# Kernel optimization log

Hardware: AMD Instinct MI355X
Metric: run time of the kernel (lower is better)

The kernel has to match this reference:

```python
import jax, jax.numpy as jnp
import numpy as np

NUM_TAGS = 256
BATCH = 64
SEQ = 512


def setup_inputs() -> dict:
    key = jax.random.key(0)
    k1, k2, k3 = jax.random.split(key, 3)
    logits = jax.random.normal(k1, (BATCH, SEQ, NUM_TAGS), dtype=jnp.float32)
    tags = jax.random.randint(k2, (BATCH, SEQ), 0, NUM_TAGS, dtype=jnp.int32)
    mask = jnp.ones((BATCH, SEQ), dtype=jnp.int32)
    # learned parameter: transitions [K, K] (xavier-normal-ish init)
    std = float(np.sqrt(2.0 / (NUM_TAGS + NUM_TAGS)))
    transitions = jax.random.normal(k3, (NUM_TAGS, NUM_TAGS), dtype=jnp.float32) * std
    return {"logits": logits, "tags": tags, "mask": mask, "transitions": transitions}


def _input_likelihood(logits, mask, transitions):
    # logits: [B, S, K], mask: [B, S] float
    logits_t = jnp.transpose(logits, (1, 0, 2))  # [S, B, K]
    mask_t = jnp.transpose(mask, (1, 0))         # [S, B]
    alpha0 = logits_t[0]                          # [B, K]

    def step(alpha, xs):
        logit_i, mask_i = xs                      # [B, K], [B]
        # inner: [B, K_prev, K_next]
        inner = alpha[:, :, None] + logit_i[:, None, :] + transitions[None, :, :]
        new_alpha = jax.nn.logsumexp(inner, axis=1)
        m = mask_i[:, None]
        alpha = new_alpha * m + alpha * (1.0 - m)
        return alpha, None

    alpha, _ = jax.lax.scan(step, alpha0, (logits_t[1:], mask_t[1:]))
    return jax.nn.logsumexp(alpha, axis=-1)      # [B]


def _joint_likelihood(logits, tags, mask, transitions):
    # logits: [B, S, K], tags: [B, S] int, mask: [B, S] float
    B, S, K = logits.shape
    # transition scores for steps 0..S-2 -> transitions[tags[i], tags[i+1]] * mask[i+1]
    trans = transitions[tags[:, :-1], tags[:, 1:]] * mask[:, 1:]      # [B, S-1]
    # emit scores for steps 0..S-2 -> logits[i, tags[i]] * mask[i]
    emit = jnp.take_along_axis(logits[:, :-1], tags[:, :-1, None], axis=-1)[..., 0] * mask[:, :-1]
    score = trans.sum(axis=1) + emit.sum(axis=1)                      # [B]
    # last valid tag per batch (mask is a contiguous prefix)
    last_idx = mask.sum(axis=1).astype(jnp.int32) - 1                 # [B]
    last_tags = jnp.take_along_axis(tags, last_idx[:, None], axis=1)[:, 0]
    last_input = logits[:, -1, :][jnp.arange(B), last_tags]           # [B]
    score = score + last_input * mask[:, -1]
    return score


def reference(logits, tags, mask, transitions):
    mask_f = mask.astype(logits.dtype)
    log_num = _joint_likelihood(logits, tags, mask_f, transitions)
    log_den = _input_likelihood(logits, mask_f, transitions)
    return jnp.sum(log_num - log_den)
```

## Files before the change

kernel.cpp:

```cpp
#include <hip/hip_runtime.h>
#include <stdint.h>

#define NTAGS 256
#define BATCH 64
#define SEQ   512
#define BR    4
#define NTHREADS 512

typedef __attribute__((ext_vector_type(8))) short short8;
typedef __attribute__((ext_vector_type(4))) float f32x4;

__device__ __forceinline__ unsigned int f32_to_bf16_bits(float f) {
  unsigned int u = __float_as_uint(f);
  return (u + 0x7FFFu + ((u >> 16) & 1u)) >> 16;
}
__device__ __forceinline__ float wave_sum(float v) {
#pragma unroll
  for (int o = 32; o; o >>= 1) v += __shfl_xor(v, o);
  return v;
}
__device__ __forceinline__ unsigned int pk_bf16(float lo, float hi) {
  unsigned int r;
  asm("v_cvt_pk_bf16_f32 %0, %1, %2" : "=v"(r) : "v"(lo), "v"(hi));
  return r;
}

#define LOG2E 1.4426950408889634f

#define BAR_LGKM() \
    asm volatile("s_waitcnt lgkmcnt(0)" ::: "memory"); \
    __builtin_amdgcn_s_barrier(); \
    asm volatile("" ::: "memory");

#define MFMA_ALL(RB) \
    f32x4 acc0 = {0.f,0.f,0.f,0.f}, acc1 = {0.f,0.f,0.f,0.f}; \
    _Pragma("unroll") \
    for (int c = 0; c < 8; ++c) { \
      const short8 bf = *(const short8*)&alds[RB][bidxs[c]]; \
      acc0 = __builtin_amdgcn_mfma_f32_16x16x32_bf16(aF[0][c], bf, acc0, 0, 0, 0); \
      acc1 = __builtin_amdgcn_mfma_f32_16x16x32_bf16(aF[1][c], bf, acc1, 0, 0, 0); \
    }

#define EPI_TILE_F(I, ACCI, PB, WB, ME) { \
      const uint2 pw = PB[I]; \
      const float p0_ = __uint_as_float(pw.x << 16); \
      const float p1_ = __uint_as_float(pw.x & 0xFFFF0000u); \
      const float p2_ = __uint_as_float(pw.y << 16); \
      const float p3_ = __uint_as_float(pw.y & 0xFFFF0000u); \
      const float n0 = (MM ? ACCI[0] * p0_ : sOld[I][0]) * sc; \
      const float n1 = (MM ? ACCI[1] * p1_ : sOld[I][1]) * sc; \
      const float n2 = (MM ? ACCI[2] * p2_ : sOld[I][2]) * sc; \
      const float n3 = (MM ? ACCI[3] * p3_ : sOld[I][3]) * sc; \
      sOld[I][0] = n0; sOld[I][1] = n1; sOld[I][2] = n2; sOld[I][3] = n3; \
      if (ME) mxl = fmaxf(mxl, fmaxf(fmaxf(n0, n1), fmaxf(n2, n3))); \
      uint2 wv; wv.x = pk_bf16(n0, n1); wv.y = pk_bf16(n2, n3); \
      if (wrt) *(uint2*)&alds[WB][widx[I]] = wv; }

#define EPI_TILE_B(I, ACCI, PB, WB, ME) { \
      const uint2 pw = PB[I]; \
      const float p0_ = __uint_as_float(pw.x << 16); \
      const float p1_ = __uint_as_float(pw.x & 0xFFFF0000u); \
      const float p2_ = __uint_as_float(pw.y << 16); \
      const float p3_ = __uint_as_float(pw.y & 0xFFFF0000u); \
      float n0, n1, n2, n3; \
      if (fastm) { \
        n0 = ACCI[0] * p0_ * sc; n1 = ACCI[1] * p1_ * sc; \
        n2 = ACCI[2] * p2_ * sc; n3 = ACCI[3] * p3_ * sc; \
      } else { \
        const float q0_ = __uint_as_float(gp[I].x << 16); \
        const float q1_ = __uint_as_float(gp[I].x & 0xFFFF0000u); \
        const float q2_ = __uint_as_float(gp[I].y << 16); \
        const float q3_ = __uint_as_float(gp[I].y & 0xFFFF0000u); \
        n0 = (MM ? ACCI[0] * p0_ : sOld[I][0] * (p0_ / q0_)) * sc; \
        n1 = (MM ? ACCI[1] * p1_ : sOld[I][1] * (p1_ / q1_)) * sc; \
        n2 = (MM ? ACCI[2] * p2_ : sOld[I][2] * (p2_ / q2_)) * sc; \
        n3 = (MM ? ACCI[3] * p3_ : sOld[I][3] * (p3_ / q3_)) * sc; \
      } \
      gp[I] = pw; \
      sOld[I][0] = n0; sOld[I][1] = n1; sOld[I][2] = n2; sOld[I][3] = n3; \
      if (ME) mxl = fmaxf(mxl, fmaxf(fmaxf(n0, n1), fmaxf(n2, n3))); \
      uint2 wv; wv.x = pk_bf16(n0, n1); wv.y = pk_bf16(n2, n3); \
      if (wrt) *(uint2*)&alds[WB][widx[I]] = wv; }

#define APPLY_BODY() { \
      const f32x4 mxa = *(const f32x4*)&maxw[pc][0]; \
      const f32x4 mxb = *(const f32x4*)&maxw[pc][4]; \
      const float mx = fmaxf(fmaxf(fmaxf(mxa[0], mxa[1]), fmaxf(mxa[2], mxa[3])), \
                             fmaxf(fmaxf(mxb[0], mxb[1]), fmaxf(mxb[2], mxb[3]))); \
      const int e = (int)((__float_as_uint(mx) >> 23) & 0xFF) - 127; \
      esum += e; \
      sc = __uint_as_float((unsigned int)(127 - e) << 23); }

#define STEPF(T, RB, WB, PC, PL, MC, ML, APPLY, MEAS) { \
    { const int tp_ = ((T) + 2 < SEQ) ? ((T) + 2) : (SEQ - 1); \
      _Pragma("unroll") \
      for (int i2 = 0; i2 < 2; ++i2) PL[i2] = *(const uint2*)(Pp + (size_t)tp_ * NTAGS + 16 * i2); \
      ML = mkp[tp_]; } \
    MFMA_ALL(RB) \
    float sc = 1.0f; \
    if (APPLY) APPLY_BODY() \
    const int MM = MC; \
    float mxl = -3.0e38f; \
    EPI_TILE_F(0, acc0, PC, WB, MEAS) EPI_TILE_F(1, acc1, PC, WB, MEAS) \
    if (MEAS) { \
      float v = mxl; v = fmaxf(v, __shfl_xor(v, 16)); v = fmaxf(v, __shfl_xor(v, 32)); \
      if (q == 0 && wrt) maxw[p][wid] = v; \
    } \
    BAR_LGKM() }

#define STEPB(T, RB, WB, PC, PL, MC, ML, APPLY, MEAS) { \
    { const int tp_ = ((T) >= 2) ? ((T) - 2) : 0; \
      const int tm_ = ((T) >= 1) ? ((T) - 1) : 0; \
      _Pragma("unroll") \
      for (int i2 = 0; i2 < 2; ++i2) PL[i2] = *(const uint2*)(Pp + (size_t)tp_ * NTAGS + 16 * i2); \
      ML = mkp[tm_]; } \
    MFMA_ALL(RB) \
    float sc = 1.0f; \
    if (APPLY) APPLY_BODY() \
    const int MM = MC; \
    const bool fastm = (bool)__all(MM != 0); \
    float mxl = -3.0e38f; \
    EPI_TILE_B(0, acc0, PC, WB, MEAS) EPI_TILE_B(1, acc1, PC, WB, MEAS) \
    if (MEAS) { \
      float v = mxl; v = fmaxf(v, __shfl_xor(v, 16)); v = fmaxf(v, __shfl_xor(v, 32)); \
      if (q == 0 && wrt) maxw[p][wid] = v; \
    } \
    BAR_LGKM() }

__global__ __launch_bounds__(256)
void crf_prep(const float* __restrict__ lg, unsigned int* __restrict__ P)
{
  const size_t g = (size_t)blockIdx.x * 256 + threadIdx.x;
  const float4 a = ((const float4*)lg)[2 * g];
  const float4 b = ((const float4*)lg)[2 * g + 1];
  uint4 o;
  o.x = pk_bf16(exp2f(a.x * LOG2E), exp2f(a.y * LOG2E));
  o.y = pk_bf16(exp2f(a.z * LOG2E), exp2f(a.w * LOG2E));
  o.z = pk_bf16(exp2f(b.x * LOG2E), exp2f(b.y * LOG2E));
  o.w = pk_bf16(exp2f(b.z * LOG2E), exp2f(b.w * LOG2E));
  ((uint4*)P)[g] = o;
}

__global__ __launch_bounds__(NTHREADS, 2)
void crf_halves(const unsigned short* __restrict__ P,
                const int*   __restrict__ mask,
                const float* __restrict__ trans,
                float* __restrict__ wsA, float* __restrict__ wsB,
                int* __restrict__ wseF, int* __restrict__ wseB)
{
  const int bid  = blockIdx.x;
  const int bwd  = bid >> 4;
  const int b0   = (bid & 15) * BR;
  const int tid  = threadIdx.x;
  const int wid  = tid >> 6;
  const int lane = tid & 63;
  const int p    = lane & 15;
  const int pc   = p & (BR - 1);
  const int q    = lane >> 4;
  const bool wrt = (p < BR);

  __shared__ __align__(16) short alds[2][NTAGS * BR];
  __shared__ __align__(32) float maxw[BR][8];

  const unsigned short* Pp = P + (size_t)(b0 + pc) * SEQ * NTAGS + 32 * wid + 4 * q;
  const int* mkp = mask + (b0 + pc) * SEQ;

  int bidxs[8], widx[2];
#pragma unroll
  for (int c = 0; c < 8; ++c) bidxs[c] = (pc * NTAGS + 32 * c + 8 * q) ^ ((pc & 1) << 5);
#pragma unroll
  for (int i = 0; i < 2; ++i) widx[i] = (p * NTAGS + 32 * wid + 16 * i + 4 * q) ^ ((p & 1) << 5);

  short8 aF[2][8];
#pragma unroll
  for (int i = 0; i < 2; ++i) {
    const int m = 32 * wid + 16 * i + p;
#pragma unroll
    for (int c = 0; c < 8; ++c) {
      short8 w;
#pragma unroll
      for (int j = 0; j < 8; ++j) {
        const int tag = 32 * c + 8 * q + j;
        const float tv = bwd ? trans[m * NTAGS + tag] : trans[tag * NTAGS + m];
        w[j] = (short)f32_to_bf16_bits(exp2f(tv * LOG2E));
      }
      aF[i][c] = w;
    }
  }

  f32x4 sOld[2];
  uint2 p0[2], p1[2], p2[2], p3[2], gp[2];
  int m0 = 1, m1 = 1, m2 = 1, m3 = 1;
  int esum = 0;

  if (!bwd) {
#pragma unroll
    for (int i = 0; i < 2; ++i) {
      const uint2 pw = *(const uint2*)(Pp + 16 * i);
      f32x4 a;
      a[0] = __uint_as_float(pw.x << 16); a[1] = __uint_as_float(pw.x & 0xFFFF0000u);
      a[2] = __uint_as_float(pw.y << 16); a[3] = __uint_as_float(pw.y & 0xFFFF0000u);
      sOld[i] = a;
      if (wrt) *(uint2*)&alds[0][widx[i]] = pw;
    }
#pragma unroll
    for (int i = 0; i < 2; ++i) {
      p1[i] = *(const uint2*)(Pp + 1 * NTAGS + 16 * i);
      p2[i] = *(const uint2*)(Pp + 2 * NTAGS + 16 * i);
    }
    m1 = mkp[1]; m2 = mkp[2];
    __syncthreads();

    STEPF(1, 0, 1, p1, p3, m1, m3, 0, 0)
    STEPF(2, 1, 0, p2, p0, m2, m0, 0, 0)
    STEPF(3, 0, 1, p3, p1, m3, m1, 0, 1)
#pragma unroll 1
    for (int tb = 4; tb <= 248; tb += 4) {
      STEPF(tb + 0, 1, 0, p0, p2, m0, m2, 1, 0)
      STEPF(tb + 1, 0, 1, p1, p3, m1, m3, 0, 0)
      STEPF(tb + 2, 1, 0, p2, p0, m2, m0, 0, 0)
      STEPF(tb + 3, 0, 1, p3, p1, m3, m1, 0, 1)
    }
    STEPF(252, 1, 0, p0, p2, m0, m2, 1, 0)
    STEPF(253, 0, 1, p1, p3, m1, m3, 0, 0)
    STEPF(254, 1, 0, p2, p0, m2, m0, 0, 0)

    {
      MFMA_ALL(0)
      const int MM = m3;
      float* wp = wsA + (size_t)(b0 + pc) * NTAGS + 32 * wid + 4 * q;
#pragma unroll
      for (int i = 0; i < 2; ++i) {
        const uint2 pw = p3[i];
        f32x4 pv;
        pv[0] = __uint_as_float(pw.x << 16); pv[1] = __uint_as_float(pw.x & 0xFFFF0000u);
        pv[2] = __uint_as_float(pw.y << 16); pv[3] = __uint_as_float(pw.y & 0xFFFF0000u);
        f32x4 o;
        const f32x4 ac = (i == 0) ? acc0 : acc1;
#pragma unroll
        for (int r = 0; r < 4; ++r)
          o[r] = MM ? ac[r] * pv[r] : sOld[i][r];
        if (wrt) *(f32x4*)(wp + 16 * i) = o;
      }
    }
    if (tid < BR) wseF[b0 + tid] = esum;
  } else {
#pragma unroll
    for (int i = 0; i < 2; ++i) {
      const uint2 pw = *(const uint2*)(Pp + (size_t)(SEQ - 1) * NTAGS + 16 * i);
      f32x4 a;
      a[0] = __uint_as_float(pw.x << 16); a[1] = __uint_as_float(pw.x & 0xFFFF0000u);
      a[2] = __uint_as_float(pw.y << 16); a[3] = __uint_as_float(pw.y & 0xFFFF0000u);
      sOld[i] = a; gp[i] = pw;
      if (wrt) *(uint2*)&alds[0][widx[i]] = pw;
    }
#pragma unroll
    for (int i = 0; i < 2; ++i) {
      p2[i] = *(const uint2*)(Pp + (size_t)510 * NTAGS + 16 * i);
      p1[i] = *(const uint2*)(Pp + (size_t)509 * NTAGS + 16 * i);
    }
    m2 = mkp[511];
    m1 = mkp[510];
    __syncthreads();

    STEPB(510, 0, 1, p2, p0, m2, m0, 0, 0)
    STEPB(509, 1, 0, p1, p3, m1, m3, 0, 0)
    STEPB(508, 0, 1, p0, p2, m0, m2, 0, 1)
#pragma unroll 1
    for (int tb = 507; tb >= 263; tb -= 4) {
      STEPB(tb - 0, 1, 0, p3, p1, m3, m1, 1, 0)
      STEPB(tb - 1, 0, 1, p2, p0, m2, m0, 0, 0)
      STEPB(tb - 2, 1, 0, p1, p3, m1, m3, 0, 0)
      STEPB(tb - 3, 0, 1, p0, p2, m0, m2, 0, 1)
    }
    STEPB(259, 1, 0, p3, p1, m3, m1, 1, 0)
    STEPB(258, 0, 1, p2, p0, m2, m0, 0, 0)
    STEPB(257, 1, 0, p1, p3, m1, m3, 0, 0)
    STEPB(256, 0, 1, p0, p2, m0, m2, 0, 0)

    {
      MFMA_ALL(1)
      float* wp = wsB + (size_t)(b0 + pc) * NTAGS + 32 * wid + 4 * q;
      if (wrt) {
        *(f32x4*)(wp + 0)  = acc0;
        *(f32x4*)(wp + 16) = acc1;
      }
    }
    if (tid < BR) wseB[b0 + tid] = esum;
  }
}

__global__ __launch_bounds__(256)
void crf_combine(const float* __restrict__ logits,
                 const int*   __restrict__ tags,
                 const int*   __restrict__ mask,
                 const float* __restrict__ trans,
                 const float* __restrict__ wsA,
                 const float* __restrict__ wsB,
                 const int*   __restrict__ wseF,
                 const int*   __restrict__ wseB,
                 float* __restrict__ out)
{
  const int b    = blockIdx.x;
  const int tid  = threadIdx.x;
  const int lane = tid & 63;
  const int wid  = tid >> 6;

  __shared__ float rn[4], rm[4], rp[4];

  const float LN2 = 0.6931471805599453f;
  const float* lg = logits + (size_t)b * SEQ * NTAGS;
  const int*   tg = tags + b * SEQ;
  const int*   mk = mask + b * SEQ;

  float numer = 0.f, msum = 0.f;
  for (int t = tid; t < SEQ; t += 256) {
    int   tag_t = tg[t];
    float m_t   = (float)mk[t];
    msum += m_t;
    if (t < SEQ - 1) {
      numer += lg[t * NTAGS + tag_t] * m_t;
      numer += trans[tag_t * NTAGS + tg[t + 1]] * (float)mk[t + 1];
    }
  }
  numer = wave_sum(numer);
  msum  = wave_sum(msum);
  if (lane == 0) { rn[wid] = numer; rm[wid] = msum; }

  float pprod = wsA[b * NTAGS + tid] * wsB[b * NTAGS + tid];
  pprod = wave_sum(pprod);
  if (lane == 0) rp[wid] = pprod;
  __syncthreads();

  if (tid == 0) {
    const float numer_tot = (rn[0] + rn[1]) + (rn[2] + rn[3]);
    const float msum_tot  = (rm[0] + rm[1]) + (rm[2] + rm[3]);
    const float psum      = (rp[0] + rp[1]) + (rp[2] + rp[3]);
    const float log_den   = logf(psum) + (float)(wseF[b] + wseB[b]) * LN2;
    int last_idx = (int)msum_tot - 1;
    if (last_idx < 0) last_idx = 0;
    const int last_tag = tg[last_idx];
    const float score = numer_tot + lg[(SEQ - 1) * NTAGS + last_tag] * (float)mk[SEQ - 1];
    atomicAdd(out, score - log_den);
  }
}

extern "C" void kernel_launch(void* const* d_in, const int* in_sizes, int n_in,
                              void* d_out, int out_size, void* d_ws, size_t ws_size,
                              hipStream_t stream) {
  const float* logits = (const float*)d_in[0];
  const int*   tags   = (const int*)d_in[1];
  const int*   mask   = (const int*)d_in[2];
  const float* trans  = (const float*)d_in[3];
  float* out = (float*)d_out;

  unsigned short* P = (unsigned short*)d_ws;
  float* wsA  = (float*)((char*)d_ws + (size_t)BATCH * SEQ * NTAGS * 2);
  float* wsB  = wsA + BATCH * NTAGS;
  int*   wseF = (int*)(wsB + BATCH * NTAGS);
  int*   wseB = wseF + BATCH;

  hipMemsetAsync(out, 0, sizeof(float), stream);
  crf_prep<<<dim3(BATCH * SEQ * NTAGS / (256 * 8)), dim3(256), 0, stream>>>(logits, (unsigned int*)P);
  crf_halves<<<dim3(32), dim3(NTHREADS), 0, stream>>>(P, mask, trans, wsA, wsB, wseF, wseB);
  crf_combine<<<dim3(BATCH), dim3(256), 0, stream>>>(logits, tags, mask, trans, wsA, wsB, wseF, wseB, out);
}
```

Before: 241.0 us.

## Give each block a single batch row, launching 128 blocks instead of 32

The recurrence kernel now assigns one batch element per block instead of four, so the grid grows from 32 to 128 blocks and more CUs work on the sequential scan in parallel. The MFMA B operand now carries only one useful column, so most of each 16-wide tile is wasted compute, and the per-block shared-memory layout and swizzle are simplified to match. The forward epilogue also gains a fast path for all-ones masks, and the rescale multiply is skipped on steps that do not apply a new scale. The trade is more total MFMA work and more repeated loads of the transition matrix in exchange for a shorter per-block critical path.

```diff
diff --git a/kernel.cpp b/kernel.cpp
--- a/kernel.cpp
+++ b/kernel.cpp
@@ -4,7 +4,6 @@
 #define NTAGS 256
 #define BATCH 64
 #define SEQ   512
-#define BR    4
 #define NTHREADS 512
 
 typedef __attribute__((ext_vector_type(8))) short short8;
@@ -41,22 +40,7 @@
       acc1 = __builtin_amdgcn_mfma_f32_16x16x32_bf16(aF[1][c], bf, acc1, 0, 0, 0); \
     }
 
-#define EPI_TILE_F(I, ACCI, PB, WB, ME) { \
-      const uint2 pw = PB[I]; \
-      const float p0_ = __uint_as_float(pw.x << 16); \
-      const float p1_ = __uint_as_float(pw.x & 0xFFFF0000u); \
-      const float p2_ = __uint_as_float(pw.y << 16); \
-      const float p3_ = __uint_as_float(pw.y & 0xFFFF0000u); \
-      const float n0 = (MM ? ACCI[0] * p0_ : sOld[I][0]) * sc; \
-      const float n1 = (MM ? ACCI[1] * p1_ : sOld[I][1]) * sc; \
-      const float n2 = (MM ? ACCI[2] * p2_ : sOld[I][2]) * sc; \
-      const float n3 = (MM ? ACCI[3] * p3_ : sOld[I][3]) * sc; \
-      sOld[I][0] = n0; sOld[I][1] = n1; sOld[I][2] = n2; sOld[I][3] = n3; \
-      if (ME) mxl = fmaxf(mxl, fmaxf(fmaxf(n0, n1), fmaxf(n2, n3))); \
-      uint2 wv; wv.x = pk_bf16(n0, n1); wv.y = pk_bf16(n2, n3); \
-      if (wrt) *(uint2*)&alds[WB][widx[I]] = wv; }
-
-#define EPI_TILE_B(I, ACCI, PB, WB, ME) { \
+#define EPI_TILE_F(I, ACCI, PB, WB, ME, AP) { \
       const uint2 pw = PB[I]; \
       const float p0_ = __uint_as_float(pw.x << 16); \
       const float p1_ = __uint_as_float(pw.x & 0xFFFF0000u); \
@@ -64,18 +48,41 @@
       const float p3_ = __uint_as_float(pw.y & 0xFFFF0000u); \
       float n0, n1, n2, n3; \
       if (fastm) { \
-        n0 = ACCI[0] * p0_ * sc; n1 = ACCI[1] * p1_ * sc; \
-        n2 = ACCI[2] * p2_ * sc; n3 = ACCI[3] * p3_ * sc; \
+        n0 = ACCI[0] * p0_; n1 = ACCI[1] * p1_; \
+        n2 = ACCI[2] * p2_; n3 = ACCI[3] * p3_; \
+      } else { \
+        n0 = MM ? ACCI[0] * p0_ : sOld[I][0]; \
+        n1 = MM ? ACCI[1] * p1_ : sOld[I][1]; \
+        n2 = MM ? ACCI[2] * p2_ : sOld[I][2]; \
+        n3 = MM ? ACCI[3] * p3_ : sOld[I][3]; \
+      } \
+      if (AP) { n0 *= sc; n1 *= sc; n2 *= sc; n3 *= sc; } \
+      sOld[I][0] = n0; sOld[I][1] = n1; sOld[I][2] = n2; sOld[I][3] = n3; \
+      if (ME) mxl = fmaxf(mxl, fmaxf(fmaxf(n0, n1), fmaxf(n2, n3))); \
+      uint2 wv; wv.x = pk_bf16(n0, n1); wv.y = pk_bf16(n2, n3); \
+      if (wrt) *(uint2*)&alds[WB][widx[I]] = wv; }
+
+#define EPI_TILE_B(I, ACCI, PB, WB, ME, AP) { \
+      const uint2 pw = PB[I]; \
+      const float p0_ = __uint_as_float(pw.x << 16); \
+      const float p1_ = __uint_as_float(pw.x & 0xFFFF0000u); \
+      const float p2_ = __uint_as_float(pw.y << 16); \
+      const float p3_ = __uint_as_float(pw.y & 0xFFFF0000u); \
+      float n0, n1, n2, n3; \
+      if (fastm) { \
+        n0 = ACCI[0] * p0_; n1 = ACCI[1] * p1_; \
+        n2 = ACCI[2] * p2_; n3 = ACCI[3] * p3_; \
       } else { \
         const float q0_ = __uint_as_float(gp[I].x << 16); \
         const float q1_ = __uint_as_float(gp[I].x & 0xFFFF0000u); \
         const float q2_ = __uint_as_float(gp[I].y << 16); \
         const float q3_ = __uint_as_float(gp[I].y & 0xFFFF0000u); \
-        n0 = (MM ? ACCI[0] * p0_ : sOld[I][0] * (p0_ / q0_)) * sc; \
-        n1 = (MM ? ACCI[1] * p1_ : sOld[I][1] * (p1_ / q1_)) * sc; \
-        n2 = (MM ? ACCI[2] * p2_ : sOld[I][2] * (p2_ / q2_)) * sc; \
-        n3 = (MM ? ACCI[3] * p3_ : sOld[I][3] * (p3_ / q3_)) * sc; \
+        n0 = MM ? ACCI[0] * p0_ : sOld[I][0] * (p0_ / q0_); \
+        n1 = MM ? ACCI[1] * p1_ : sOld[I][1] * (p1_ / q1_); \
+        n2 = MM ? ACCI[2] * p2_ : sOld[I][2] * (p2_ / q2_); \
+        n3 = MM ? ACCI[3] * p3_ : sOld[I][3] * (p3_ / q3_); \
       } \
+      if (AP) { n0 *= sc; n1 *= sc; n2 *= sc; n3 *= sc; } \
       gp[I] = pw; \
       sOld[I][0] = n0; sOld[I][1] = n1; sOld[I][2] = n2; sOld[I][3] = n3; \
       if (ME) mxl = fmaxf(mxl, fmaxf(fmaxf(n0, n1), fmaxf(n2, n3))); \
@@ -83,8 +90,8 @@
       if (wrt) *(uint2*)&alds[WB][widx[I]] = wv; }
 
 #define APPLY_BODY() { \
-      const f32x4 mxa = *(const f32x4*)&maxw[pc][0]; \
-      const f32x4 mxb = *(const f32x4*)&maxw[pc][4]; \
+      const f32x4 mxa = *(const f32x4*)&maxw[0]; \
+      const f32x4 mxb = *(const f32x4*)&maxw[4]; \
       const float mx = fmaxf(fmaxf(fmaxf(mxa[0], mxa[1]), fmaxf(mxa[2], mxa[3])), \
                              fmaxf(fmaxf(mxb[0], mxb[1]), fmaxf(mxb[2], mxb[3]))); \
       const int e = (int)((__float_as_uint(mx) >> 23) & 0xFF) - 127; \
@@ -100,11 +107,12 @@
     float sc = 1.0f; \
     if (APPLY) APPLY_BODY() \
     const int MM = MC; \
+    const bool fastm = (bool)__all(MM != 0); \
     float mxl = -3.0e38f; \
-    EPI_TILE_F(0, acc0, PC, WB, MEAS) EPI_TILE_F(1, acc1, PC, WB, MEAS) \
+    EPI_TILE_F(0, acc0, PC, WB, MEAS, APPLY) EPI_TILE_F(1, acc1, PC, WB, MEAS, APPLY) \
     if (MEAS) { \
       float v = mxl; v = fmaxf(v, __shfl_xor(v, 16)); v = fmaxf(v, __shfl_xor(v, 32)); \
-      if (q == 0 && wrt) maxw[p][wid] = v; \
+      if (q == 0 && wrt) maxw[wid] = v; \
     } \
     BAR_LGKM() }
 
@@ -120,10 +128,10 @@
     const int MM = MC; \
     const bool fastm = (bool)__all(MM != 0); \
     float mxl = -3.0e38f; \
-    EPI_TILE_B(0, acc0, PC, WB, MEAS) EPI_TILE_B(1, acc1, PC, WB, MEAS) \
+    EPI_TILE_B(0, acc0, PC, WB, MEAS, APPLY) EPI_TILE_B(1, acc1, PC, WB, MEAS, APPLY) \
     if (MEAS) { \
       float v = mxl; v = fmaxf(v, __shfl_xor(v, 16)); v = fmaxf(v, __shfl_xor(v, 32)); \
-      if (q == 0 && wrt) maxw[p][wid] = v; \
+      if (q == 0 && wrt) maxw[wid] = v; \
     } \
     BAR_LGKM() }
 
@@ -149,27 +157,26 @@
                 int* __restrict__ wseF, int* __restrict__ wseB)
 {
   const int bid  = blockIdx.x;
-  const int bwd  = bid >> 4;
-  const int b0   = (bid & 15) * BR;
+  const int bwd  = bid >> 6;
+  const int b    = bid & 63;
   const int tid  = threadIdx.x;
   const int wid  = tid >> 6;
   const int lane = tid & 63;
   const int p    = lane & 15;
-  const int pc   = p & (BR - 1);
   const int q    = lane >> 4;
-  const bool wrt = (p < BR);
-
-  __shared__ __align__(16) short alds[2][NTAGS * BR];
-  __shared__ __align__(32) float maxw[BR][8];
-
-  const unsigned short* Pp = P + (size_t)(b0 + pc) * SEQ * NTAGS + 32 * wid + 4 * q;
-  const int* mkp = mask + (b0 + pc) * SEQ;
+  const bool wrt = (p == 0);
+
+  __shared__ __align__(16) short alds[2][NTAGS];
+  __shared__ __align__(32) float maxw[8];
+
+  const unsigned short* Pp = P + (size_t)b * SEQ * NTAGS + 32 * wid + 4 * q;
+  const int* mkp = mask + b * SEQ;
 
   int bidxs[8], widx[2];
 #pragma unroll
-  for (int c = 0; c < 8; ++c) bidxs[c] = (pc * NTAGS + 32 * c + 8 * q) ^ ((pc & 1) << 5);
-#pragma unroll
-  for (int i = 0; i < 2; ++i) widx[i] = (p * NTAGS + 32 * wid + 16 * i + 4 * q) ^ ((p & 1) << 5);
+  for (int c = 0; c < 8; ++c) bidxs[c] = 32 * c + 8 * q;
+#pragma unroll
+  for (int i = 0; i < 2; ++i) widx[i] = 32 * wid + 16 * i + 4 * q;
 
   short8 aF[2][8];
 #pragma unroll
@@ -228,7 +235,7 @@
     {
       MFMA_ALL(0)
       const int MM = m3;
-      float* wp = wsA + (size_t)(b0 + pc) * NTAGS + 32 * wid + 4 * q;
+      float* wp = wsA + (size_t)b * NTAGS + 32 * wid + 4 * q;
 #pragma unroll
       for (int i = 0; i < 2; ++i) {
         const uint2 pw = p3[i];
@@ -243,7 +250,7 @@
         if (wrt) *(f32x4*)(wp + 16 * i) = o;
       }
     }
-    if (tid < BR) wseF[b0 + tid] = esum;
+    if (tid == 0) wseF[b] = esum;
   } else {
 #pragma unroll
     for (int i = 0; i < 2; ++i) {
@@ -280,13 +287,13 @@
 
     {
       MFMA_ALL(1)
-      float* wp = wsB + (size_t)(b0 + pc) * NTAGS + 32 * wid + 4 * q;
+      float* wp = wsB + (size_t)b * NTAGS + 32 * wid + 4 * q;
       if (wrt) {
         *(f32x4*)(wp + 0)  = acc0;
         *(f32x4*)(wp + 16) = acc1;
       }
     }
-    if (tid < BR) wseB[b0 + tid] = esum;
+    if (tid == 0) wseB[b] = esum;
   }
 }
 
@@ -362,6 +369,6 @@
 
   hipMemsetAsync(out, 0, sizeof(float), stream);
   crf_prep<<<dim3(BATCH * SEQ * NTAGS / (256 * 8)), dim3(256), 0, stream>>>(logits, (unsigned int*)P);
-  crf_halves<<<dim3(32), dim3(NTHREADS), 0, stream>>>(P, mask, trans, wsA, wsB, wseF, wseB);
+  crf_halves<<<dim3(128), dim3(NTHREADS), 0, stream>>>(P, mask, trans, wsA, wsB, wseF, wseB);
   crf_combine<<<dim3(BATCH), dim3(256), 0, stream>>>(logits, tags, mask, trans, wsA, wsB, wseF, wseB, out);
 }
```

After: 237.8 us. About the same (-1.3%).
